# Kernel optimization log

Hardware: AMD Instinct MI355X
Metric: run time of the kernel (lower is better)

The kernel has to match this reference:

```python
import jax, jax.numpy as jnp
import numpy as np
from jax import lax

MIN_SIZE = 25.0          # box_area threshold
IOU_THRESH = 0.3
MAX_DET = 100            # max_detections_per_image
NUM_CLASSES = 91         # COCO label space


def setup_inputs() -> dict:
    key = jax.random.key(0)
    k1, k2, k3, k4, k5 = jax.random.split(key, 5)
    B, N, H, W = 4, 1000, 256, 256
    # Realistic boxes inside a 256x256 image: centers + sizes -> xyxy.
    cxy = jax.random.uniform(k1, (B, N, 2), dtype=jnp.float32) * 256.0
    wh = jax.random.uniform(k2, (B, N, 2), dtype=jnp.float32) * 64.0 + 1.0
    boxes = jnp.concatenate([cxy - wh / 2.0, cxy + wh / 2.0], axis=-1)
    masks = jax.random.uniform(k3, (B, N, 1, H, W), dtype=jnp.float32)
    scores = jax.random.uniform(k4, (B, N), dtype=jnp.float32)
    labels = jax.random.randint(k5, (B, N), 0, NUM_CLASSES).astype(jnp.int64)
    return {"boxes": boxes, "masks": masks, "scores": scores, "labels": labels}


def _post_process_one(boxes, masks, scores, labels):
    """boxes [N,4], masks [N,1,H,W], scores [N], labels [N] -> padded top-MAX_DET."""
    N = boxes.shape[0]
    area = (boxes[:, 2] - boxes[:, 0]) * (boxes[:, 3] - boxes[:, 1])
    valid = area > MIN_SIZE                      # box_area filter

    # Sort by score descending, invalid boxes pushed to the end.
    s_masked = jnp.where(valid, scores, -jnp.inf)
    order = jnp.argsort(-s_masked)               # [N]
    b_s = boxes[order]
    a_s = area[order]
    valid_s = valid[order]

    # Pairwise IoU on sorted boxes ([N,N] ~ 4 MB for N=1000).
    lt = jnp.maximum(b_s[:, None, :2], b_s[None, :, :2])
    rb = jnp.minimum(b_s[:, None, 2:], b_s[None, :, 2:])
    wh = jnp.clip(rb - lt, 0.0)
    inter = wh[..., 0] * wh[..., 1]
    denom = a_s[:, None] + a_s[None, :] - inter
    iou = jnp.where(denom > 0.0, inter / denom, 0.0)

    idx = jnp.arange(N)

    def body(i, suppressed):
        keep_i = valid_s[i] & ~suppressed[i]
        return suppressed | (keep_i & (iou[i] > IOU_THRESH) & (idx > i))

    suppressed = lax.fori_loop(0, N, body, jnp.zeros((N,), jnp.bool_))
    keep = valid_s & ~suppressed                 # greedy NMS survivors, in score order

    # First MAX_DET kept (already score-sorted), padded with fill N.
    sel = jnp.nonzero(keep, size=MAX_DET, fill_value=N)[0]
    out_valid = sel < N
    fi = order[jnp.minimum(sel, N - 1)]          # indices into original arrays

    boxes_o = jnp.where(out_valid[:, None], boxes[fi], 0.0)
    masks_o = jnp.where(out_valid[:, None, None, None], masks[fi], 0.0)
    scores_o = jnp.where(out_valid, scores[fi], 0.0)
    labels_o = jnp.where(out_valid, labels[fi], -1)
    return boxes_o, masks_o, scores_o, labels_o, out_valid


def reference(boxes, masks, scores, labels):
    # vmap over the batch: [B,100,4], [B,100,1,H,W], [B,100], [B,100], [B,100]
    return jax.vmap(_post_process_one)(boxes, masks, scores, labels)
```

## Files before the change

### kernel.cpp

```cpp
#include <hip/hip_runtime.h>
#include <cstdint>
#include <cstddef>

#define NB 4
#define NN 1000
#define NPAD 1024
#define HW 65536
#define MAXDET 100
#define MIN_SIZE 25.0f
#define IOU_T 0.3f
#define PARTS 4
#define PART_F4 (HW / 4 / PARTS)

#define OFF_BOXES  0
#define OFF_MASKS  (NB * MAXDET * 4)
#define OFF_SCORES (OFF_MASKS + (size_t)NB * MAXDET * HW)
#define OFF_LABELS (OFF_SCORES + NB * MAXDET)
#define OFF_VALID  (OFF_LABELS + NB * MAXDET)

__global__ __launch_bounds__(256) void nms_kernel(
    const float* __restrict__ boxes,
    const float* __restrict__ scores,
    const int*   __restrict__ labels,
    float* __restrict__ out,
    int*   __restrict__ sel)
{
    __shared__ float s_score[NPAD];
    __shared__ int   s_idx[NPAD];
    __shared__ float sx1[NPAD], sy1[NPAD], sx2[NPAD], sy2[NPAD], sar[NPAD];
    __shared__ int   alive[NPAD];
    __shared__ int   s_scan[256];

    const int b   = blockIdx.x;
    const int tid = threadIdx.x;
    const float* bboxes  = boxes  + (size_t)b * NN * 4;
    const float* bscores = scores + (size_t)b * NN;
    const int*   blabels = labels + (size_t)b * NN;

    for (int e = tid; e < NPAD; e += 256) {
        float sc = -INFINITY;
        if (e < NN) {
            float x1 = bboxes[e * 4 + 0], y1 = bboxes[e * 4 + 1];
            float x2 = bboxes[e * 4 + 2], y2 = bboxes[e * 4 + 3];
            float area = (x2 - x1) * (y2 - y1);
            if (area > MIN_SIZE) sc = bscores[e];
        }
        s_score[e] = sc;
        s_idx[e]   = e;
    }
    __syncthreads();

    for (int k = 2; k <= NPAD; k <<= 1) {
        for (int j = k >> 1; j > 0; j >>= 1) {
            for (int e = tid; e < NPAD; e += 256) {
                int ixj = e ^ j;
                if (ixj > e) {
                    float sa = s_score[e], sb = s_score[ixj];
                    int   ia = s_idx[e],   ib = s_idx[ixj];
                    bool a_first = (sa > sb) || (sa == sb && ia < ib);
                    bool up = ((e & k) == 0);
                    if (up ? !a_first : a_first) {
                        s_score[e] = sb; s_score[ixj] = sa;
                        s_idx[e]   = ib; s_idx[ixj]   = ia;
                    }
                }
            }
            __syncthreads();
        }
    }

    for (int e = tid; e < NPAD; e += 256) {
        int fi = s_idx[e];
        float x1 = 0.f, y1 = 0.f, x2 = 0.f, y2 = 0.f, area = 0.f;
        int al = 0;
        if (fi < NN) {
            x1 = bboxes[fi * 4 + 0]; y1 = bboxes[fi * 4 + 1];
            x2 = bboxes[fi * 4 + 2]; y2 = bboxes[fi * 4 + 3];
            area = (x2 - x1) * (y2 - y1);
            al = (area > MIN_SIZE) ? 1 : 0;
        }
        sx1[e] = x1; sy1[e] = y1; sx2[e] = x2; sy2[e] = y2; sar[e] = area;
        alive[e] = al;
    }
    __syncthreads();

    for (int i = 0; i < NN; ++i) {
        if (alive[i]) {
            float ix1 = sx1[i], iy1 = sy1[i], ix2 = sx2[i], iy2 = sy2[i];
            float ia = sar[i];
            for (int j = i + 1 + tid; j < NN; j += 256) {
                float ltx = fmaxf(ix1, sx1[j]);
                float lty = fmaxf(iy1, sy1[j]);
                float rbx = fminf(ix2, sx2[j]);
                float rby = fminf(iy2, sy2[j]);
                float w = fmaxf(rbx - ltx, 0.0f);
                float h = fmaxf(rby - lty, 0.0f);
                float inter = w * h;
                float denom = ia + sar[j] - inter;
                float iou = (denom > 0.0f) ? (inter / denom) : 0.0f;
                if (iou > IOU_T) alive[j] = 0;
            }
            __syncthreads();
        }
    }

    int base = tid * 4;
    int l0 = alive[base + 0], l1 = alive[base + 1];
    int l2 = alive[base + 2], l3 = alive[base + 3];
    int lsum = l0 + l1 + l2 + l3;
    s_scan[tid] = lsum;
    __syncthreads();
    for (int off = 1; off < 256; off <<= 1) {
        int v = (tid >= off) ? s_scan[tid - off] : 0;
        __syncthreads();
        s_scan[tid] += v;
        __syncthreads();
    }
    int total = s_scan[255];
    int r = s_scan[tid] - lsum;

    float* out_boxes  = out + OFF_BOXES;
    float* out_scores = out + OFF_SCORES;
    float* out_labels = out + OFF_LABELS;
    float* out_valid  = out + OFF_VALID;

    #pragma unroll
    for (int q = 0; q < 4; ++q) {
        int al = (q == 0) ? l0 : (q == 1) ? l1 : (q == 2) ? l2 : l3;
        if (al) {
            if (r < MAXDET) {
                int e = base + q;
                int fi = s_idx[e];
                int slot = b * MAXDET + r;
                sel[slot] = fi;
                out_boxes[slot * 4 + 0] = bboxes[fi * 4 + 0];
                out_boxes[slot * 4 + 1] = bboxes[fi * 4 + 1];
                out_boxes[slot * 4 + 2] = bboxes[fi * 4 + 2];
                out_boxes[slot * 4 + 3] = bboxes[fi * 4 + 3];
                out_scores[slot] = bscores[fi];
                out_labels[slot] = (float)blabels[fi];
                out_valid[slot]  = 1.0f;
            }
            r++;
        }
    }

    int count = (total < MAXDET) ? total : MAXDET;
    for (int k2 = tid; k2 < MAXDET; k2 += 256) {
        if (k2 >= count) {
            int slot = b * MAXDET + k2;
            sel[slot] = -1;
            out_boxes[slot * 4 + 0] = 0.0f;
            out_boxes[slot * 4 + 1] = 0.0f;
            out_boxes[slot * 4 + 2] = 0.0f;
            out_boxes[slot * 4 + 3] = 0.0f;
            out_scores[slot] = 0.0f;
            out_labels[slot] = -1.0f;
            out_valid[slot]  = 0.0f;
        }
    }
}

__global__ __launch_bounds__(256) void gather_masks(
    const float* __restrict__ masks,
    const int*   __restrict__ sel,
    float* __restrict__ out_masks)
{
    int blk  = blockIdx.x;
    int slot = blk / PARTS;
    int part = blk % PARTS;
    int b    = slot / MAXDET;
    int fi   = sel[slot];

    float4* dst = (float4*)out_masks + (size_t)slot * (HW / 4) + (size_t)part * PART_F4;
    if (fi >= 0) {
        const float4* src = (const float4*)masks
                          + (size_t)(b * NN + fi) * (HW / 4) + (size_t)part * PART_F4;
        for (int t = threadIdx.x; t < PART_F4; t += 256) dst[t] = src[t];
    } else {
        float4 z = make_float4(0.f, 0.f, 0.f, 0.f);
        for (int t = threadIdx.x; t < PART_F4; t += 256) dst[t] = z;
    }
}

extern "C" void kernel_launch(void* const* d_in, const int* in_sizes, int n_in,
                              void* d_out, int out_size, void* d_ws, size_t ws_size,
                              hipStream_t stream) {
    const float* boxes  = (const float*)d_in[0];
    const float* masks  = (const float*)d_in[1];
    const float* scores = (const float*)d_in[2];
    const int*   labels = (const int*)d_in[3];
    float* out = (float*)d_out;
    int*   sel = (int*)d_ws;

    nms_kernel<<<NB, 256, 0, stream>>>(boxes, scores, labels, out, sel);
    gather_masks<<<NB * MAXDET * PARTS, 256, 0, stream>>>(masks, sel, out + OFF_MASKS);
}
```

Baseline: 1.489 ms.

## Rewrite NMS as parallel IoU bitmask plus single-wave greedy suppression scan

Replaces the serial per-box suppression loop, which needed a block barrier per alive box, with a precomputed upper-triangular IoU bitmask. The 64x64 tiles of that bitmask are built in parallel by 16 waves and stored in workspace. A single wavefront then walks the rows and ORs in the suppression masks, prefetching rows from global memory. The kernel also moves to 1024 threads per block, uses a ballot-based compaction for ranking, and splits the mask gather across twice as many blocks. The cost is extra global traffic for zeroing and reading the mask, plus a serial single-wave scan.

New measurement: 1.440 ms. 3.3% less time.

```diff
diff --git a/kernel.cpp b/kernel.cpp
--- a/kernel.cpp
+++ b/kernel.cpp
@@ -9,7 +9,7 @@
 #define MAXDET 100
 #define MIN_SIZE 25.0f
 #define IOU_T 0.3f
-#define PARTS 4
+#define PARTS 8
 #define PART_F4 (HW / 4 / PARTS)
 
 #define OFF_BOXES  0
@@ -18,146 +18,181 @@
 #define OFF_LABELS (OFF_SCORES + NB * MAXDET)
 #define OFF_VALID  (OFF_LABELS + NB * MAXDET)
 
-__global__ __launch_bounds__(256) void nms_kernel(
+#define WS_MASK_OFF 2048
+
+__global__ __launch_bounds__(1024) void nms_all(
     const float* __restrict__ boxes,
     const float* __restrict__ scores,
     const int*   __restrict__ labels,
     float* __restrict__ out,
-    int*   __restrict__ sel)
+    int*   __restrict__ sel,
+    unsigned long long* __restrict__ g_mask_all)
 {
-    __shared__ float s_score[NPAD];
-    __shared__ int   s_idx[NPAD];
-    __shared__ float sx1[NPAD], sy1[NPAD], sx2[NPAD], sy2[NPAD], sar[NPAD];
-    __shared__ int   alive[NPAD];
-    __shared__ int   s_scan[256];
+    __shared__ float  s_score[NPAD];
+    __shared__ int    s_idx[NPAD];
+    __shared__ float4 s_box[NPAD];
+    __shared__ float  s_area[NPAD];
+    __shared__ unsigned long long s_validbits[16];
+    __shared__ unsigned long long s_sup[16];
+    __shared__ int    s_wsum[16];
+    __shared__ int    s_woff[17];
 
     const int b   = blockIdx.x;
     const int tid = threadIdx.x;
-    const float* bboxes  = boxes  + (size_t)b * NN * 4;
-    const float* bscores = scores + (size_t)b * NN;
-    const int*   blabels = labels + (size_t)b * NN;
-
-    for (int e = tid; e < NPAD; e += 256) {
+    const int wv  = tid >> 6;
+    const int lane = tid & 63;
+
+    const float4* bb4   = (const float4*)(boxes + (size_t)b * NN * 4);
+    const float*  bsc   = scores + (size_t)b * NN;
+    const int*    blb   = labels + (size_t)b * NN;
+    unsigned long long* gm = g_mask_all + (size_t)b * NN * 16;
+
+    {
         float sc = -INFINITY;
-        if (e < NN) {
-            float x1 = bboxes[e * 4 + 0], y1 = bboxes[e * 4 + 1];
-            float x2 = bboxes[e * 4 + 2], y2 = bboxes[e * 4 + 3];
-            float area = (x2 - x1) * (y2 - y1);
-            if (area > MIN_SIZE) sc = bscores[e];
-        }
-        s_score[e] = sc;
-        s_idx[e]   = e;
-    }
-    __syncthreads();
+        if (tid < NN) {
+            float4 v = bb4[tid];
+            float a = (v.z - v.x) * (v.w - v.y);
+            if (a > MIN_SIZE) sc = bsc[tid];
+        }
+        s_score[tid] = sc;
+        s_idx[tid]   = tid;
+        for (int t = tid; t < NN * 16; t += 1024) gm[t] = 0ull;
+    }
 
     for (int k = 2; k <= NPAD; k <<= 1) {
         for (int j = k >> 1; j > 0; j >>= 1) {
-            for (int e = tid; e < NPAD; e += 256) {
-                int ixj = e ^ j;
-                if (ixj > e) {
-                    float sa = s_score[e], sb = s_score[ixj];
-                    int   ia = s_idx[e],   ib = s_idx[ixj];
-                    bool a_first = (sa > sb) || (sa == sb && ia < ib);
-                    bool up = ((e & k) == 0);
-                    if (up ? !a_first : a_first) {
-                        s_score[e] = sb; s_score[ixj] = sa;
-                        s_idx[e]   = ib; s_idx[ixj]   = ia;
-                    }
+            __syncthreads();
+            int ixj = tid ^ j;
+            if (ixj > tid) {
+                float sa = s_score[tid], sb = s_score[ixj];
+                int   ia = s_idx[tid],   ib = s_idx[ixj];
+                bool a_first = (sa > sb) || (sa == sb && ia < ib);
+                bool up = ((tid & k) == 0);
+                if (up ? !a_first : a_first) {
+                    s_score[tid] = sb; s_score[ixj] = sa;
+                    s_idx[tid]   = ib; s_idx[ixj]   = ia;
                 }
             }
-            __syncthreads();
-        }
-    }
-
-    for (int e = tid; e < NPAD; e += 256) {
-        int fi = s_idx[e];
-        float x1 = 0.f, y1 = 0.f, x2 = 0.f, y2 = 0.f, area = 0.f;
-        int al = 0;
+        }
+    }
+    __syncthreads();
+
+    {
+        int fi = s_idx[tid];
+        float4 bx = make_float4(0.f, 0.f, 0.f, 0.f);
+        float ar = 0.f;
+        bool val = false;
         if (fi < NN) {
-            x1 = bboxes[fi * 4 + 0]; y1 = bboxes[fi * 4 + 1];
-            x2 = bboxes[fi * 4 + 2]; y2 = bboxes[fi * 4 + 3];
-            area = (x2 - x1) * (y2 - y1);
-            al = (area > MIN_SIZE) ? 1 : 0;
-        }
-        sx1[e] = x1; sy1[e] = y1; sx2[e] = x2; sy2[e] = y2; sar[e] = area;
-        alive[e] = al;
-    }
-    __syncthreads();
-
-    for (int i = 0; i < NN; ++i) {
-        if (alive[i]) {
-            float ix1 = sx1[i], iy1 = sy1[i], ix2 = sx2[i], iy2 = sy2[i];
-            float ia = sar[i];
-            for (int j = i + 1 + tid; j < NN; j += 256) {
-                float ltx = fmaxf(ix1, sx1[j]);
-                float lty = fmaxf(iy1, sy1[j]);
-                float rbx = fminf(ix2, sx2[j]);
-                float rby = fminf(iy2, sy2[j]);
-                float w = fmaxf(rbx - ltx, 0.0f);
-                float h = fmaxf(rby - lty, 0.0f);
-                float inter = w * h;
-                float denom = ia + sar[j] - inter;
-                float iou = (denom > 0.0f) ? (inter / denom) : 0.0f;
-                if (iou > IOU_T) alive[j] = 0;
+            bx = bb4[fi];
+            ar = (bx.z - bx.x) * (bx.w - bx.y);
+            val = ar > MIN_SIZE;
+        }
+        s_box[tid] = bx;
+        s_area[tid] = ar;
+        unsigned long long vb = __ballot(val);
+        if (lane == 0) s_validbits[wv] = vb;
+    }
+    __syncthreads();
+
+    for (int p = wv; p < 136; p += 16) {
+        int rb = 0, base = 0;
+        while (base + 16 - rb <= p) { base += 16 - rb; ++rb; }
+        int w = rb + (p - base);
+        int i = (rb << 6) + lane;
+        float4 bi = s_box[i];
+        float  ai = s_area[i];
+        unsigned long long m = 0ull;
+        int jb = w << 6;
+        for (int j2 = 0; j2 < 64; ++j2) {
+            int j = jb + j2;
+            float4 bj = s_box[j];
+            float  aj = s_area[j];
+            float ltx = fmaxf(bi.x, bj.x);
+            float lty = fmaxf(bi.y, bj.y);
+            float rbx = fminf(bi.z, bj.z);
+            float rby = fminf(bi.w, bj.w);
+            float cw = fmaxf(rbx - ltx, 0.0f);
+            float ch = fmaxf(rby - lty, 0.0f);
+            float inter = cw * ch;
+            float den = ai + aj - inter;
+            float iou = (den > 0.0f) ? (inter / den) : 0.0f;
+            m |= (unsigned long long)((iou > IOU_T) && (j > i)) << j2;
+        }
+        if (i < NN) gm[(size_t)i * 16 + w] = m;
+    }
+    __syncthreads();
+
+    if (tid < 64) {
+        const bool lw = lane < 16;
+        unsigned long long sup = 0ull;
+        unsigned long long pre0 = lw ? gm[(size_t)0 * 16 + lane] : 0ull;
+        unsigned long long pre1 = lw ? gm[(size_t)1 * 16 + lane] : 0ull;
+        unsigned long long pre2 = lw ? gm[(size_t)2 * 16 + lane] : 0ull;
+        unsigned long long pre3 = lw ? gm[(size_t)3 * 16 + lane] : 0ull;
+        for (int c = 0; c < 16; ++c) {
+            unsigned long long supw = __shfl(sup, c);
+            unsigned long long vw = s_validbits[c];
+            const int nb = (c == 15) ? (NN - 15 * 64) : 64;
+            for (int bit = 0; bit < nb; bit += 4) {
+#define STEP(PH, B) { \
+                int i = (c << 6) + bit + (B); \
+                unsigned long long row = PH; \
+                int nx = i + 4; if (nx >= NN) nx = NN - 1; \
+                PH = lw ? gm[(size_t)nx * 16 + lane] : 0ull; \
+                if (((vw >> (bit + (B))) & 1ull) && !((supw >> (bit + (B))) & 1ull)) { \
+                    sup |= row; \
+                    supw = __shfl(sup, c); \
+                } }
+                STEP(pre0, 0)
+                STEP(pre1, 1)
+                STEP(pre2, 2)
+                STEP(pre3, 3)
+#undef STEP
             }
-            __syncthreads();
-        }
-    }
-
-    int base = tid * 4;
-    int l0 = alive[base + 0], l1 = alive[base + 1];
-    int l2 = alive[base + 2], l3 = alive[base + 3];
-    int lsum = l0 + l1 + l2 + l3;
-    s_scan[tid] = lsum;
-    __syncthreads();
-    for (int off = 1; off < 256; off <<= 1) {
-        int v = (tid >= off) ? s_scan[tid - off] : 0;
-        __syncthreads();
-        s_scan[tid] += v;
-        __syncthreads();
-    }
-    int total = s_scan[255];
-    int r = s_scan[tid] - lsum;
+        }
+        if (lw) s_sup[lane] = sup;
+    }
+    __syncthreads();
+
+    unsigned long long vwd = s_validbits[wv];
+    unsigned long long swd = s_sup[wv];
+    bool kp = (((vwd >> lane) & 1ull) != 0) && (((swd >> lane) & 1ull) == 0);
+    unsigned long long bal = __ballot(kp);
+    int lprefix = __popcll(bal & ((1ull << lane) - 1ull));
+    if (lane == 0) s_wsum[wv] = __popcll(bal);
+    __syncthreads();
+    if (tid == 0) {
+        int s = 0;
+        for (int q = 0; q < 16; ++q) { s_woff[q] = s; s += s_wsum[q]; }
+        s_woff[16] = s;
+    }
+    __syncthreads();
+    int rank  = s_woff[wv] + lprefix;
+    int total = s_woff[16];
 
     float* out_boxes  = out + OFF_BOXES;
     float* out_scores = out + OFF_SCORES;
     float* out_labels = out + OFF_LABELS;
     float* out_valid  = out + OFF_VALID;
-
-    #pragma unroll
-    for (int q = 0; q < 4; ++q) {
-        int al = (q == 0) ? l0 : (q == 1) ? l1 : (q == 2) ? l2 : l3;
-        if (al) {
-            if (r < MAXDET) {
-                int e = base + q;
-                int fi = s_idx[e];
-                int slot = b * MAXDET + r;
-                sel[slot] = fi;
-                out_boxes[slot * 4 + 0] = bboxes[fi * 4 + 0];
-                out_boxes[slot * 4 + 1] = bboxes[fi * 4 + 1];
-                out_boxes[slot * 4 + 2] = bboxes[fi * 4 + 2];
-                out_boxes[slot * 4 + 3] = bboxes[fi * 4 + 3];
-                out_scores[slot] = bscores[fi];
-                out_labels[slot] = (float)blabels[fi];
-                out_valid[slot]  = 1.0f;
-            }
-            r++;
-        }
-    }
-
-    int count = (total < MAXDET) ? total : MAXDET;
-    for (int k2 = tid; k2 < MAXDET; k2 += 256) {
-        if (k2 >= count) {
-            int slot = b * MAXDET + k2;
-            sel[slot] = -1;
-            out_boxes[slot * 4 + 0] = 0.0f;
-            out_boxes[slot * 4 + 1] = 0.0f;
-            out_boxes[slot * 4 + 2] = 0.0f;
-            out_boxes[slot * 4 + 3] = 0.0f;
-            out_scores[slot] = 0.0f;
-            out_labels[slot] = -1.0f;
-            out_valid[slot]  = 0.0f;
-        }
+    const int slot_base = b * MAXDET;
+
+    if (kp && rank < MAXDET) {
+        int slot = slot_base + rank;
+        int fi = s_idx[tid];
+        sel[slot] = fi;
+        ((float4*)out_boxes)[slot] = s_box[tid];
+        out_scores[slot] = s_score[tid];
+        out_labels[slot] = (float)blb[fi];
+        out_valid[slot]  = 1.0f;
+    }
+    int count = total < MAXDET ? total : MAXDET;
+    if (tid >= count && tid < MAXDET) {
+        int slot = slot_base + tid;
+        sel[slot] = -1;
+        ((float4*)out_boxes)[slot] = make_float4(0.f, 0.f, 0.f, 0.f);
+        out_scores[slot] = 0.0f;
+        out_labels[slot] = -1.0f;
+        out_valid[slot]  = 0.0f;
     }
 }
 
@@ -192,7 +227,8 @@
     const int*   labels = (const int*)d_in[3];
     float* out = (float*)d_out;
     int*   sel = (int*)d_ws;
-
-    nms_kernel<<<NB, 256, 0, stream>>>(boxes, scores, labels, out, sel);
+    unsigned long long* g_mask = (unsigned long long*)((char*)d_ws + WS_MASK_OFF);
+
+    nms_all<<<NB, 1024, 0, stream>>>(boxes, scores, labels, out, sel, g_mask);
     gather_masks<<<NB * MAXDET * PARTS, 256, 0, stream>>>(masks, sel, out + OFF_MASKS);
 }
```
